# Performance work log

Hardware: AMD Instinct MI355X
Metric: run time of the kernel (lower is better)

Reference implementation:

```python
import jax, jax.numpy as jnp
import numpy as np

N_NODES = 65536
IN_CH = 512
HIDDEN = 256          # hidden_channels[0] == encoder_hidden
OUT_CH = 8
NUM_GRAPHS = 32
MAX_LEN = 4096        # static pad bound (>= max per-graph length)
BN_EPS = 1e-5


def _make_batch_ids():
    # deterministic ragged per-graph lengths summing exactly to N_NODES
    rng = np.random.RandomState(0)
    d = rng.randint(-512, 512, size=NUM_GRAPHS)
    d[-1] -= d.sum()
    lengths = N_NODES // NUM_GRAPHS + d          # each in ~[1536, 2560] <= MAX_LEN
    return jnp.asarray(np.repeat(np.arange(NUM_GRAPHS), lengths), dtype=jnp.int32)


def setup_inputs() -> dict:
    key = jax.random.key(0)
    ks = jax.random.split(key, 12)
    f32 = jnp.float32
    inp = {
        'x_res': jax.random.normal(ks[0], (N_NODES, IN_CH), dtype=f32),
        'batch': _make_batch_ids(),
        # BatchNorm1d affine params
        'bn_gamma': jnp.ones((IN_CH,), f32),
        'bn_beta': jnp.zeros((IN_CH,), f32),
        # input2transformer: Linear(C,2H) GELU Linear(2H,H) GELU Linear(H,H)
        'W1': jax.random.normal(ks[1], (IN_CH, 2 * HIDDEN), f32) * (1.0 / np.sqrt(IN_CH)),
        'b1': jnp.zeros((2 * HIDDEN,), f32),
        'W2': jax.random.normal(ks[2], (2 * HIDDEN, HIDDEN), f32) * (1.0 / np.sqrt(2 * HIDDEN)),
        'b2': jnp.zeros((HIDDEN,), f32),
        'W3': jax.random.normal(ks[3], (HIDDEN, HIDDEN), f32) * (1.0 / np.sqrt(HIDDEN)),
        'b3': jnp.zeros((HIDDEN,), f32),
        # out_angles: Linear(encoder_hidden, out_ch) GELU DynamicTanh Tanh
        'Wo': jax.random.normal(ks[4], (HIDDEN, OUT_CH), f32) * (1.0 / np.sqrt(HIDDEN)),
        'bo': jnp.zeros((OUT_CH,), f32),
        'dyt_alpha': jnp.asarray(0.5, f32),
        'dyt_w': jnp.ones((OUT_CH,), f32),
        'dyt_b': jnp.zeros((OUT_CH,), f32),
    }
    return inp


def _forward(x_res, batch, bn_gamma, bn_beta, W1, b1, W2, b2, W3, b3,
             Wo, bo, dyt_alpha, dyt_w, dyt_b):
    # BatchNorm1d (training-mode batch stats, biased var), dropout is identity (eval)
    mu = jnp.mean(x_res, axis=0)
    var = jnp.mean((x_res - mu) ** 2, axis=0)
    x = (x_res - mu) * jax.lax.rsqrt(var + BN_EPS) * bn_gamma + bn_beta
    # input2transformer MLP (torch GELU default = exact erf)
    gelu = lambda t: jax.nn.gelu(t, approximate=False)
    x = gelu(x @ W1 + b1)
    x = gelu(x @ W2 + b2)
    x = x @ W3 + b3                                   # [N, HIDDEN]
    # ragged -> padded: scatter each node into (graph, position-in-graph)
    counts = jax.ops.segment_sum(jnp.ones_like(batch, dtype=jnp.int32), batch,
                                 num_segments=NUM_GRAPHS)
    offsets = jnp.concatenate([jnp.zeros((1,), jnp.int32),
                               jnp.cumsum(counts)[:-1].astype(jnp.int32)])
    pos = jnp.arange(N_NODES, dtype=jnp.int32) - offsets[batch]
    x_pad = jnp.zeros((NUM_GRAPHS, MAX_LEN, HIDDEN), x.dtype).at[batch, pos].set(x)
    z = jnp.transpose(x_pad, (1, 0, 2))               # [MAX_LEN, NUM_GRAPHS, HIDDEN] (stack dim=1)
    # out_angles head: Linear -> GELU -> DynamicTanh -> Tanh
    a = gelu(z @ Wo + bo)
    a = dyt_w * jnp.tanh(dyt_alpha * a) + dyt_b       # DynamicTanh (channels_last)
    return jnp.tanh(a)                                # [MAX_LEN, NUM_GRAPHS, OUT_CH]


def reference(x_res, batch, bn_gamma, bn_beta, W1, b1, W2, b2, W3, b3,
              Wo, bo, dyt_alpha, dyt_w, dyt_b):
    return _forward(x_res, batch, bn_gamma, bn_beta, W1, b1, W2, b2, W3, b3,
                    Wo, bo, dyt_alpha, dyt_w, dyt_b)
```

## Files before the change

kernel.cpp:

```cpp
#include <hip/hip_runtime.h>
#include <hip/hip_bf16.h>

#define N_NODES 65536
#define IN_CH 512
#define HIDDEN 256
#define OUT_CH 8
#define NUM_GRAPHS 32
#define MAX_LEN 4096
#define BN_EPS 1e-5f
#define BN_BLOCKS 2048

using short8  = __attribute__((ext_vector_type(8))) short;
using floatx4 = __attribute__((ext_vector_type(4))) float;
typedef unsigned int u32;
typedef unsigned short u16;

__device__ inline u16 f2b(float f) {
    u32 u = __float_as_uint(f);
    u += 0x7FFFu + ((u >> 16) & 1u);
    return (u16)(u >> 16);
}
__device__ inline float gelu_f(float x) {
    float z = x + 0.044715f * x * x * x;
    float e = __builtin_exp2f(-2.3022078f * z);
    return x * __builtin_amdgcn_rcpf(1.0f + e);
}
__device__ inline float tanh_f(float y) {
    y = fminf(fmaxf(y, -20.0f), 20.0f);
    float t = __builtin_exp2f(2.885390082f * y);
    return (t - 1.0f) * __builtin_amdgcn_rcpf(t + 1.0f);
}
__device__ inline void load_lds16(const void* g, void* l) {
    __builtin_amdgcn_global_load_lds(
        (const __attribute__((address_space(1))) u32*)g,
        (__attribute__((address_space(3))) u32*)l, 16, 0, 0);
}

__global__ __launch_bounds__(256) void statscast_k(const float* __restrict__ x,
                                                   u16* __restrict__ xb,
                                                   float4* __restrict__ partials) {
    __shared__ float4 sS[128];
    __shared__ float4 sQ[128];
    int tid = threadIdx.x;
    int half = tid >> 7;
    int c = tid & 127;
    const float4* x4 = (const float4*)x;
    uint2* xb2 = (uint2*)xb;
    float4 s = make_float4(0.f, 0.f, 0.f, 0.f);
    float4 q = make_float4(0.f, 0.f, 0.f, 0.f);
    int row0 = blockIdx.x * 32;
#pragma unroll
    for (int r = half; r < 32; r += 2) {
        size_t off = (size_t)(row0 + r) * 128 + c;
        float4 v = x4[off];
        s.x += v.x; s.y += v.y; s.z += v.z; s.w += v.w;
        q.x += v.x * v.x; q.y += v.y * v.y; q.z += v.z * v.z; q.w += v.w * v.w;
        uint2 o;
        o.x = (u32)f2b(v.x) | ((u32)f2b(v.y) << 16);
        o.y = (u32)f2b(v.z) | ((u32)f2b(v.w) << 16);
        xb2[off] = o;
    }
    if (half == 1) { sS[c] = s; sQ[c] = q; }
    __syncthreads();
    if (half == 0) {
        float4 s2 = sS[c], q2 = sQ[c];
        s.x += s2.x; s.y += s2.y; s.z += s2.z; s.w += s2.w;
        q.x += q2.x; q.y += q2.y; q.z += q2.z; q.w += q2.w;
        partials[(size_t)blockIdx.x * 256 + c * 2]     = make_float4(s.x, q.x, s.y, q.y);
        partials[(size_t)blockIdx.x * 256 + c * 2 + 1] = make_float4(s.z, q.z, s.w, q.w);
    }
}

__global__ __launch_bounds__(256) void bn_reduce_k(const float4* __restrict__ partials,
                                                   const float* __restrict__ gamma,
                                                   const float* __restrict__ beta,
                                                   float* __restrict__ scale,
                                                   float* __restrict__ shift) {
    __shared__ float4 sd[256];
    int tid = threadIdx.x;
    int g = blockIdx.x;
    float4 a = make_float4(0.f, 0.f, 0.f, 0.f);
    for (int r = tid; r < BN_BLOCKS; r += 256) {
        float4 v = partials[(size_t)r * 256 + g];
        a.x += v.x; a.y += v.y; a.z += v.z; a.w += v.w;
    }
    sd[tid] = a;
    __syncthreads();
    for (int st = 128; st > 0; st >>= 1) {
        if (tid < st) {
            float4 b = sd[tid + st];
            float4 m = sd[tid];
            m.x += b.x; m.y += b.y; m.z += b.z; m.w += b.w;
            sd[tid] = m;
        }
        __syncthreads();
    }
    if (tid == 0) {
        float4 t = sd[0];
        int c0 = g * 2, c1 = g * 2 + 1;
        const float inv = 1.0f / N_NODES;
        float mu0 = t.x * inv, var0 = t.y * inv - mu0 * mu0;
        float mu1 = t.z * inv, var1 = t.w * inv - mu1 * mu1;
        float sc0 = gamma[c0] * rsqrtf(var0 + BN_EPS);
        float sc1 = gamma[c1] * rsqrtf(var1 + BN_EPS);
        scale[c0] = sc0; shift[c0] = beta[c0] - mu0 * sc0;
        scale[c1] = sc1; shift[c1] = beta[c1] - mu1 * sc1;
    }
}

__global__ __launch_bounds__(256) void prep_k(const float* __restrict__ W1,
                                              const float* __restrict__ W2,
                                              const float* __restrict__ W3,
                                              const float* __restrict__ b1,
                                              const float* __restrict__ scale,
                                              const float* __restrict__ shift,
                                              u16* __restrict__ W1T,
                                              u16* __restrict__ W2T,
                                              u16* __restrict__ W3T,
                                              float* __restrict__ b1f,
                                              const int* __restrict__ batch,
                                              int* __restrict__ offsets,
                                              const float* __restrict__ bo,
                                              const float* __restrict__ alpha_p,
                                              const float* __restrict__ dyt_w,
                                              const float* __restrict__ dyt_b,
                                              float* __restrict__ out) {
    __shared__ int sof2[NUM_GRAPHS + 1];
    int bid = blockIdx.x;
    int tid = threadIdx.x;
    if (bid < 1792) {
        int idx = bid * 256 + tid;
        if (idx < 262144) {
            int k = idx >> 9, m = idx & 511;
            W1T[(size_t)m * 512 + k] = f2b(scale[k] * W1[idx]);
        } else if (idx < 262144 + 131072) {
            int i = idx - 262144;
            int k = i >> 8, m = i & 255;
            W2T[(size_t)m * 512 + k] = f2b(W2[i]);
        } else {
            int i = idx - 393216;
            int k = i >> 8, m = i & 255;
            W3T[(size_t)m * 256 + k] = f2b(W3[i]);
        }
        if (bid == 0 && tid < NUM_GRAPHS + 1) {
            int gph = tid;
            int lo = 0, hi = N_NODES;
            while (lo < hi) {
                int mid = (lo + hi) >> 1;
                if (batch[mid] < gph) lo = mid + 1; else hi = mid;
            }
            offsets[gph] = lo;
        }
    } else if (bid < 1794) {
        int m = (bid - 1792) * 256 + tid;
        float acc = b1[m];
#pragma unroll 16
        for (int k = 0; k < 512; ++k) acc += shift[k] * W1[k * 512 + m];
        b1f[m] = acc;
    } else {
        if (tid < NUM_GRAPHS + 1) {
            int target = tid;
            int lo = 0, hi = N_NODES;
            while (lo < hi) {
                int mid = (lo + hi) >> 1;
                if (batch[mid] < target) lo = mid + 1; else hi = mid;
            }
            sof2[tid] = lo;
        }
        __syncthreads();
        int idx = (bid - 1794) * 256 + tid;
        int g = idx & 31;
        int p = idx >> 5;
        if (p >= sof2[g + 1] - sof2[g]) {
            float alpha = alpha_p[0];
            float rv[8];
#pragma unroll
            for (int c = 0; c < 8; ++c) {
                float a = gelu_f(bo[c]);
                a = dyt_w[c] * tanh_f(alpha * a) + dyt_b[c];
                rv[c] = tanh_f(a);
            }
            float4* o = (float4*)(out + (size_t)idx * OUT_CH);
            o[0] = make_float4(rv[0], rv[1], rv[2], rv[3]);
            o[1] = make_float4(rv[4], rv[5], rv[6], rv[7]);
        }
    }
}

template <int DO_GELU, int NXB>
__global__ __launch_bounds__(512) void gemm_bt_k(const u16* __restrict__ A,
                                                 const u16* __restrict__ BT,
                                                 const float* __restrict__ bias,
                                                 u16* __restrict__ C,
                                                 int K, int M) {
    __shared__ __align__(16) u16 As[256 * 64];
    __shared__ __align__(16) u16 Bs[128 * 64];
    int tid = threadIdx.x;
    int lane = tid & 63;
    int bid = blockIdx.x;
    int xcd = bid & 7;
    int slot = bid >> 3;
    int rloc = slot / NXB;
    int colb = slot - rloc * NXB;
    int row0 = (xcd * 32 + rloc) * 256;
    int col0 = colb * 128;
    int wave = tid >> 6;
    int wr = (wave >> 1) * 64;
    int wc = (wave & 1) * 64;
    int l15 = lane & 15;
    int q = lane >> 4;

    floatx4 acc[4][4] = {};

    const int nkt = K >> 6;
    for (int kt = 0; kt < nkt; ++kt) {
        int k0 = kt << 6;
#pragma unroll
        for (int s = 0; s < 4; ++s) {
            int li = s * 512 + tid;
            int r = li >> 3;
            int g = li & 7;
            int gs = g ^ (r & 7);
            load_lds16(&A[(size_t)(row0 + r) * K + k0 + gs * 8], &As[li * 8]);
        }
#pragma unroll
        for (int s = 0; s < 2; ++s) {
            int li = s * 512 + tid;
            int r = li >> 3;
            int g = li & 7;
            int gs = g ^ (r & 7);
            load_lds16(&BT[(size_t)(col0 + r) * K + k0 + gs * 8], &Bs[li * 8]);
        }
        __syncthreads();
#pragma unroll
        for (int ks = 0; ks < 2; ++ks) {
            int gidx = ks * 4 + q;
            short8 af[4], bg[4];
#pragma unroll
            for (int i = 0; i < 4; ++i) {
                int row = wr + i * 16 + l15;
                af[i] = *(const short8*)&As[row * 64 + (gidx ^ (row & 7)) * 8];
            }
#pragma unroll
            for (int j = 0; j < 4; ++j) {
                int row = wc + j * 16 + l15;
                bg[j] = *(const short8*)&Bs[row * 64 + (gidx ^ (row & 7)) * 8];
            }
#pragma unroll
            for (int i = 0; i < 4; ++i)
#pragma unroll
                for (int j = 0; j < 4; ++j)
                    acc[i][j] = __builtin_amdgcn_mfma_f32_16x16x32_bf16(bg[j], af[i], acc[i][j], 0, 0, 0);
        }
        __syncthreads();
    }
#pragma unroll
    for (int i = 0; i < 4; ++i) {
        size_t rbase = (size_t)(row0 + wr + i * 16 + l15) * M;
#pragma unroll
        for (int j = 0; j < 4; ++j) {
            int c = col0 + wc + j * 16 + q * 4;
            float4 b4 = *(const float4*)&bias[c];
            float v0 = acc[i][j][0] + b4.x;
            float v1 = acc[i][j][1] + b4.y;
            float v2 = acc[i][j][2] + b4.z;
            float v3 = acc[i][j][3] + b4.w;
            if (DO_GELU) { v0 = gelu_f(v0); v1 = gelu_f(v1); v2 = gelu_f(v2); v3 = gelu_f(v3); }
            uint2 pk;
            pk.x = (u32)f2b(v0) | ((u32)f2b(v1) << 16);
            pk.y = (u32)f2b(v2) | ((u32)f2b(v3) << 16);
            *(uint2*)&C[rbase + c] = pk;
        }
    }
}

#define FENCE asm volatile("" ::: "memory")

__global__ __launch_bounds__(512, 2) void gemm23h_k(const u16* __restrict__ A,
                                                    const u16* __restrict__ B2T,
                                                    const float* __restrict__ b2v,
                                                    const u16* __restrict__ W3T,
                                                    const float* __restrict__ b3v,
                                                    const float* __restrict__ Wo,
                                                    const float* __restrict__ bo,
                                                    const int* __restrict__ offsets,
                                                    const float* __restrict__ alpha_p,
                                                    const float* __restrict__ dyt_w,
                                                    const float* __restrict__ dyt_b,
                                                    float* __restrict__ out) {
    __shared__ __align__(16) u16 lds[65536];
    __shared__ float sWo[HIDDEN * OUT_CH];
    __shared__ int soff[NUM_GRAPHS + 1];
    int tid = threadIdx.x;
    int lane = tid & 63;
    int bid = blockIdx.x;
    int xcd = bid & 7;
    int slot = bid >> 3;
    int row0 = (xcd * 32 + slot) * 256;
    int wave = tid >> 6;
    int wr = (wave >> 2) * 128;
    int wc = (wave & 3) * 64;
    int l15 = lane & 15;
    int q = lane >> 4;

    ((float4*)sWo)[tid] = ((const float4*)Wo)[tid];
    if (tid < NUM_GRAPHS + 1) soff[tid] = offsets[tid];

    floatx4 acc[8][4] = {};

    const u16* pA[4];
    const u16* pB[4];
    int ldst[4];
#pragma unroll
    for (int s = 0; s < 4; ++s) {
        int li = s * 512 + tid;
        int r = li >> 3;
        int g = li & 7;
        int gs = g ^ (r & 7);
        pA[s] = A + (size_t)(row0 + r) * 512 + gs * 8;
        pB[s] = B2T + (size_t)r * 512 + gs * 8;
        ldst[s] = li * 8;
    }

#define LDA2(BASE, GIDX)                                                             \
    _Pragma("unroll")                                                                \
    for (int i = 0; i < 4; ++i) {                                                    \
        int row = (BASE) + i * 16 + l15;                                             \
        af[i] = *(const short8*)&lds[curA + row * 64 + (((GIDX) ^ (row & 7)) << 3)]; \
    }
#define LDB2(BASE, GIDX)                                                             \
    _Pragma("unroll")                                                                \
    for (int j = 0; j < 4; ++j) {                                                    \
        int row = (BASE) + j * 16 + l15;                                             \
        bg[j] = *(const short8*)&lds[curB + row * 64 + (((GIDX) ^ (row & 7)) << 3)]; \
    }
#define MFMA16(IB)                                                                   \
    __builtin_amdgcn_s_setprio(1);                                                   \
    _Pragma("unroll")                                                                \
    for (int i = 0; i < 4; ++i)                                                      \
        _Pragma("unroll")                                                            \
        for (int j = 0; j < 4; ++j)                                                  \
            acc[(IB) + i][j] = __builtin_amdgcn_mfma_f32_16x16x32_bf16(              \
                bg[j], af[i], acc[(IB) + i][j], 0, 0, 0);                            \
    __builtin_amdgcn_s_setprio(0)

#pragma unroll
    for (int s = 0; s < 4; ++s) load_lds16(pA[s], &lds[ldst[s]]);
#pragma unroll
    for (int s = 0; s < 4; ++s) load_lds16(pB[s], &lds[32768 + ldst[s]]);

    const int nt = 8;
    for (int t = 0; t < nt; ++t) {
        const int cur = t & 1;
        const int nx = cur ^ 1;
        const bool last = (t + 1 == nt);
        const int kn = (t + 1) << 6;
        const int curA = cur * 16384, curB = 32768 + cur * 16384;
        const int nxA = nx * 16384,  nxB = 32768 + nx * 16384;
        short8 af[4], bg[4];

        if (!last) {
            load_lds16(pA[0] + kn, &lds[nxA + ldst[0]]);
            load_lds16(pA[1] + kn, &lds[nxA + ldst[1]]);
        }
        if (last) asm volatile("s_waitcnt vmcnt(0)" ::: "memory");
        else      asm volatile("s_waitcnt vmcnt(2)" ::: "memory");
        __builtin_amdgcn_s_barrier();
        FENCE;
        LDA2(wr, q);
        LDB2(wc, q);
        MFMA16(0);
        FENCE;
        __builtin_amdgcn_s_barrier();
        LDA2(wr + 64, q);
        if (!last) {
            load_lds16(pA[2] + kn, &lds[nxA + ldst[2]]);
            load_lds16(pA[3] + kn, &lds[nxA + ldst[3]]);
        }
        FENCE;
        __builtin_amdgcn_s_barrier();
        FENCE;
        MFMA16(4);
        FENCE;
        __builtin_amdgcn_s_barrier();
        LDA2(wr, 4 + q);
        LDB2(wc, 4 + q);
        if (!last) {
            load_lds16(pB[0] + kn, &lds[nxB + ldst[0]]);
            load_lds16(pB[1] + kn, &lds[nxB + ldst[1]]);
        }
        FENCE;
        __builtin_amdgcn_s_barrier();
        FENCE;
        MFMA16(0);
        FENCE;
        __builtin_amdgcn_s_barrier();
        LDA2(wr + 64, 4 + q);
        if (!last) {
            load_lds16(pB[2] + kn, &lds[nxB + ldst[2]]);
            load_lds16(pB[3] + kn, &lds[nxB + ldst[3]]);
        }
        FENCE;
        __builtin_amdgcn_s_barrier();
        FENCE;
        MFMA16(4);
        FENCE;
        __builtin_amdgcn_s_barrier();
        FENCE;
    }
    __syncthreads();

#pragma unroll
    for (int i = 0; i < 8; ++i) {
        int row = wr + i * 16 + l15;
#pragma unroll
        for (int j = 0; j < 4; ++j) {
            int c = wc + j * 16 + q * 4;
            float4 b4 = *(const float4*)&b2v[c];
            float v0 = gelu_f(acc[i][j][0] + b4.x);
            float v1 = gelu_f(acc[i][j][1] + b4.y);
            float v2 = gelu_f(acc[i][j][2] + b4.z);
            float v3 = gelu_f(acc[i][j][3] + b4.w);
            uint2 pk;
            pk.x = (u32)f2b(v0) | ((u32)f2b(v1) << 16);
            pk.y = (u32)f2b(v2) | ((u32)f2b(v3) << 16);
            int gr = c >> 3;
            int addr = row * 256 + ((gr ^ (row & 7)) << 3) + (q & 1) * 4;
            *(uint2*)&lds[addr] = pk;
        }
    }
    __syncthreads();

#pragma unroll
    for (int i = 0; i < 8; ++i)
#pragma unroll
        for (int j = 0; j < 4; ++j)
            acc[i][j] = (floatx4){0.f, 0.f, 0.f, 0.f};

    for (int ks = 0; ks < 8; ++ks) {
        int gidx = ks * 4 + q;
        short8 af[8], bg[4];
#pragma unroll
        for (int j = 0; j < 4; ++j) {
            int colr = wc + j * 16 + l15;
            bg[j] = *(const short8*)&W3T[(size_t)colr * 256 + gidx * 8];
        }
#pragma unroll
        for (int i = 0; i < 8; ++i) {
            int row = wr + i * 16 + l15;
            af[i] = *(const short8*)&lds[row * 256 + ((gidx ^ (row & 7)) << 3)];
        }
        __builtin_amdgcn_s_setprio(1);
#pragma unroll
        for (int i = 0; i < 8; ++i)
#pragma unroll
            for (int j = 0; j < 4; ++j)
                acc[i][j] = __builtin_amdgcn_mfma_f32_16x16x32_bf16(bg[j], af[i], acc[i][j], 0, 0, 0);
        __builtin_amdgcn_s_setprio(0);
    }
    __syncthreads();

#pragma unroll
    for (int i = 0; i < 8; ++i) {
        int row = wr + i * 16 + l15;
#pragma unroll
        for (int j = 0; j < 4; ++j) {
            int c = wc + j * 16 + q * 4;
            float4 b4 = *(const float4*)&b3v[c];
            float v0 = acc[i][j][0] + b4.x;
            float v1 = acc[i][j][1] + b4.y;
            float v2 = acc[i][j][2] + b4.z;
            float v3 = acc[i][j][3] + b4.w;
            uint2 pk;
            pk.x = (u32)f2b(v0) | ((u32)f2b(v1) << 16);
            pk.y = (u32)f2b(v2) | ((u32)f2b(v3) << 16);
            int gr = c >> 3;
            int addr = row * 256 + ((gr ^ (row & 31)) << 3) + (q & 1) * 4;
            *(uint2*)&lds[addr] = pk;
        }
    }
    __syncthreads();

    {
        int r = tid >> 1;
        int chalf = (tid & 1) * 4;
        int n = row0 + r;
        int lo = 0, hi = NUM_GRAPHS;
        while (hi - lo > 1) {
            int mid = (lo + hi) >> 1;
            if (soff[mid] <= n) lo = mid; else hi = mid;
        }
        int g = lo;
        int p = n - soff[g];
        float4 a4 = *(const float4*)&bo[chalf];
#pragma unroll 4
        for (int kk = 0; kk < 32; ++kk) {
            short8 h = *(const short8*)&lds[r * 256 + ((kk ^ (r & 31)) << 3)];
#pragma unroll
            for (int e = 0; e < 8; ++e) {
                float hv = __uint_as_float((u32)(u16)h[e] << 16);
                const float* w = &sWo[(kk * 8 + e) * 8 + chalf];
                a4.x += hv * w[0];
                a4.y += hv * w[1];
                a4.z += hv * w[2];
                a4.w += hv * w[3];
            }
        }
        float alpha = alpha_p[0];
        float av[4] = {a4.x, a4.y, a4.z, a4.w};
        float rv[4];
#pragma unroll
        for (int c = 0; c < 4; ++c) {
            float a = gelu_f(av[c]);
            a = dyt_w[chalf + c] * tanh_f(alpha * a) + dyt_b[chalf + c];
            rv[c] = tanh_f(a);
        }
        *(float4*)&out[((size_t)(p * NUM_GRAPHS + g)) * 8 + chalf] =
            make_float4(rv[0], rv[1], rv[2], rv[3]);
    }
#undef LDA2
#undef LDB2
#undef MFMA16
}

extern "C" void kernel_launch(void* const* d_in, const int* in_sizes, int n_in,
                              void* d_out, int out_size, void* d_ws, size_t ws_size,
                              hipStream_t stream) {
    (void)in_sizes; (void)n_in; (void)out_size; (void)ws_size;
    const float* x_res = (const float*)d_in[0];
    const int*   batch = (const int*)d_in[1];
    const float* gamma = (const float*)d_in[2];
    const float* beta  = (const float*)d_in[3];
    const float* W1    = (const float*)d_in[4];
    const float* b1    = (const float*)d_in[5];
    const float* W2    = (const float*)d_in[6];
    const float* b2    = (const float*)d_in[7];
    const float* W3    = (const float*)d_in[8];
    const float* b3    = (const float*)d_in[9];
    const float* Wo    = (const float*)d_in[10];
    const float* bo    = (const float*)d_in[11];
    const float* alpha = (const float*)d_in[12];
    const float* dyt_w = (const float*)d_in[13];
    const float* dyt_b = (const float*)d_in[14];
    float* out = (float*)d_out;

    char* ws = (char*)d_ws;
    float* scale = (float*)(ws + 0);
    float* shift = (float*)(ws + 2048);
    float* b1f   = (float*)(ws + 4096);
    int*   offs  = (int*)(ws + 8192);
    u16* W1T = (u16*)(ws + 16384);
    u16* W2T = (u16*)(ws + 16384 + 524288);
    u16* W3T = (u16*)(ws + 16384 + 524288 + 262144);
    const size_t MB = 1024 * 1024;
    u16* xb = (u16*)(ws + 2 * MB);
    u16* h1 = (u16*)(ws + 66 * MB);
    float4* partials = (float4*)(ws + 66 * MB);

    statscast_k<<<BN_BLOCKS, 256, 0, stream>>>(x_res, xb, partials);
    bn_reduce_k<<<256, 256, 0, stream>>>(partials, gamma, beta, scale, shift);
    prep_k<<<2306, 256, 0, stream>>>(W1, W2, W3, b1, scale, shift,
                                     W1T, W2T, W3T, b1f, batch, offs,
                                     bo, alpha, dyt_w, dyt_b, out);
    gemm_bt_k<1, 4><<<1024, 512, 0, stream>>>(xb, W1T, b1f, h1, 512, 512);
    gemm23h_k<<<256, 512, 0, stream>>>(h1, W2T, b2, W3T, b3, Wo, bo, offs,
                                       alpha, dyt_w, dyt_b, out);
}
```

Before: 353.2 us.

## Rewrite first GEMM with 256x256 tiles and double-buffered LDS prefetch pipeline

The first MLP GEMM (x@W1 with GELU) moves from a 256x128 tile with a single LDS buffer to a 256x256 tile with double-buffered LDS. Global-to-LDS loads for the next K tile are interleaved with MFMA phases using explicit waitcnt, barriers and setprio. This targets exposed global load latency and gives each block more operand reuse. In exchange it uses 128KB of LDS and 32 accumulators per thread, halves the grid to 512 blocks, and adds more barriers per K step.

```diff
diff --git a/kernel.cpp b/kernel.cpp
--- a/kernel.cpp
+++ b/kernel.cpp
@@ -187,14 +187,16 @@
     }
 }
 
+#define FENCE asm volatile("" ::: "memory")
+
 template <int DO_GELU, int NXB>
-__global__ __launch_bounds__(512) void gemm_bt_k(const u16* __restrict__ A,
-                                                 const u16* __restrict__ BT,
-                                                 const float* __restrict__ bias,
-                                                 u16* __restrict__ C,
-                                                 int K, int M) {
-    __shared__ __align__(16) u16 As[256 * 64];
-    __shared__ __align__(16) u16 Bs[128 * 64];
+__global__ __launch_bounds__(512, 2) void gemm_bt8_k(const u16* __restrict__ A,
+                                                     const u16* __restrict__ BT,
+                                                     const float* __restrict__ bias,
+                                                     u16* __restrict__ C,
+                                                     int K, int M) {
+    __shared__ __align__(16) u16 As[2][256 * 64];
+    __shared__ __align__(16) u16 Bs[2][256 * 64];
     int tid = threadIdx.x;
     int lane = tid & 63;
     int bid = blockIdx.x;
@@ -203,59 +205,107 @@
     int rloc = slot / NXB;
     int colb = slot - rloc * NXB;
     int row0 = (xcd * 32 + rloc) * 256;
-    int col0 = colb * 128;
+    int col0 = colb * 256;
     int wave = tid >> 6;
-    int wr = (wave >> 1) * 64;
-    int wc = (wave & 1) * 64;
+    int wr = (wave >> 2) * 128;
+    int wc = (wave & 3) * 64;
     int l15 = lane & 15;
     int q = lane >> 4;
 
-    floatx4 acc[4][4] = {};
-
-    const int nkt = K >> 6;
-    for (int kt = 0; kt < nkt; ++kt) {
-        int k0 = kt << 6;
-#pragma unroll
-        for (int s = 0; s < 4; ++s) {
-            int li = s * 512 + tid;
-            int r = li >> 3;
-            int g = li & 7;
-            int gs = g ^ (r & 7);
-            load_lds16(&A[(size_t)(row0 + r) * K + k0 + gs * 8], &As[li * 8]);
-        }
-#pragma unroll
-        for (int s = 0; s < 2; ++s) {
-            int li = s * 512 + tid;
-            int r = li >> 3;
-            int g = li & 7;
-            int gs = g ^ (r & 7);
-            load_lds16(&BT[(size_t)(col0 + r) * K + k0 + gs * 8], &Bs[li * 8]);
-        }
-        __syncthreads();
-#pragma unroll
-        for (int ks = 0; ks < 2; ++ks) {
-            int gidx = ks * 4 + q;
-            short8 af[4], bg[4];
-#pragma unroll
-            for (int i = 0; i < 4; ++i) {
-                int row = wr + i * 16 + l15;
-                af[i] = *(const short8*)&As[row * 64 + (gidx ^ (row & 7)) * 8];
-            }
-#pragma unroll
-            for (int j = 0; j < 4; ++j) {
-                int row = wc + j * 16 + l15;
-                bg[j] = *(const short8*)&Bs[row * 64 + (gidx ^ (row & 7)) * 8];
-            }
-#pragma unroll
-            for (int i = 0; i < 4; ++i)
-#pragma unroll
-                for (int j = 0; j < 4; ++j)
-                    acc[i][j] = __builtin_amdgcn_mfma_f32_16x16x32_bf16(bg[j], af[i], acc[i][j], 0, 0, 0);
-        }
-        __syncthreads();
-    }
-#pragma unroll
-    for (int i = 0; i < 4; ++i) {
+    floatx4 acc[8][4] = {};
+
+    const u16* pA[4];
+    const u16* pB[4];
+    int ldst[4];
+#pragma unroll
+    for (int s = 0; s < 4; ++s) {
+        int li = s * 512 + tid;
+        int r = li >> 3;
+        int g = li & 7;
+        int gs = g ^ (r & 7);
+        pA[s] = A + (size_t)(row0 + r) * K + gs * 8;
+        pB[s] = BT + (size_t)(col0 + r) * K + gs * 8;
+        ldst[s] = li * 8;
+    }
+
+#define LOAD_AF(BASE, GIDX)                                                    \
+    _Pragma("unroll")                                                          \
+    for (int i = 0; i < 4; ++i) {                                              \
+        int row = (BASE) + i * 16 + l15;                                       \
+        af[i] = *(const short8*)&As[cur][row * 64 + ((GIDX) ^ (row & 7)) * 8]; \
+    }
+#define LOAD_BG(BASE, GIDX)                                                    \
+    _Pragma("unroll")                                                          \
+    for (int j = 0; j < 4; ++j) {                                              \
+        int row = (BASE) + j * 16 + l15;                                       \
+        bg[j] = *(const short8*)&Bs[cur][row * 64 + ((GIDX) ^ (row & 7)) * 8]; \
+    }
+#define MFMA16(IB)                                                             \
+    __builtin_amdgcn_s_setprio(1);                                             \
+    _Pragma("unroll")                                                          \
+    for (int i = 0; i < 4; ++i)                                                \
+        _Pragma("unroll")                                                      \
+        for (int j = 0; j < 4; ++j)                                            \
+            acc[(IB) + i][j] = __builtin_amdgcn_mfma_f32_16x16x32_bf16(        \
+                bg[j], af[i], acc[(IB) + i][j], 0, 0, 0);                      \
+    __builtin_amdgcn_s_setprio(0)
+
+#pragma unroll
+    for (int s = 0; s < 4; ++s) load_lds16(pA[s], &As[0][ldst[s]]);
+#pragma unroll
+    for (int s = 0; s < 4; ++s) load_lds16(pB[s], &Bs[0][ldst[s]]);
+
+    const int nt = K >> 6;
+    for (int t = 0; t < nt; ++t) {
+        const int cur = t & 1;
+        const int nx = cur ^ 1;
+        const int kn = (t + 1 < nt) ? ((t + 1) << 6) : 0;
+        short8 af[4], bg[4];
+
+        load_lds16(pA[0] + kn, &As[nx][ldst[0]]);
+        load_lds16(pA[1] + kn, &As[nx][ldst[1]]);
+        asm volatile("s_waitcnt vmcnt(2)" ::: "memory");
+        __builtin_amdgcn_s_barrier();
+        FENCE;
+        LOAD_AF(wr, q);
+        LOAD_BG(wc, q);
+        MFMA16(0);
+        FENCE;
+        __builtin_amdgcn_s_barrier();
+        LOAD_AF(wr + 64, q);
+        load_lds16(pA[2] + kn, &As[nx][ldst[2]]);
+        load_lds16(pA[3] + kn, &As[nx][ldst[3]]);
+        FENCE;
+        __builtin_amdgcn_s_barrier();
+        FENCE;
+        MFMA16(4);
+        FENCE;
+        __builtin_amdgcn_s_barrier();
+        LOAD_AF(wr, 4 + q);
+        LOAD_BG(wc, 4 + q);
+        load_lds16(pB[0] + kn, &Bs[nx][ldst[0]]);
+        load_lds16(pB[1] + kn, &Bs[nx][ldst[1]]);
+        FENCE;
+        __builtin_amdgcn_s_barrier();
+        FENCE;
+        MFMA16(0);
+        FENCE;
+        __builtin_amdgcn_s_barrier();
+        LOAD_AF(wr + 64, 4 + q);
+        load_lds16(pB[2] + kn, &Bs[nx][ldst[2]]);
+        load_lds16(pB[3] + kn, &Bs[nx][ldst[3]]);
+        FENCE;
+        __builtin_amdgcn_s_barrier();
+        FENCE;
+        MFMA16(4);
+        FENCE;
+        __builtin_amdgcn_s_barrier();
+        FENCE;
+    }
+    asm volatile("s_waitcnt vmcnt(0)" ::: "memory");
+
+#pragma unroll
+    for (int i = 0; i < 8; ++i) {
         size_t rbase = (size_t)(row0 + wr + i * 16 + l15) * M;
 #pragma unroll
         for (int j = 0; j < 4; ++j) {
@@ -272,9 +322,10 @@
             *(uint2*)&C[rbase + c] = pk;
         }
     }
-}
-
-#define FENCE asm volatile("" ::: "memory")
+#undef LOAD_AF
+#undef LOAD_BG
+#undef MFMA16
+}
 
 __global__ __launch_bounds__(512, 2) void gemm23h_k(const u16* __restrict__ A,
                                                     const u16* __restrict__ B2T,
@@ -562,7 +613,7 @@
     prep_k<<<2306, 256, 0, stream>>>(W1, W2, W3, b1, scale, shift,
                                      W1T, W2T, W3T, b1f, batch, offs,
                                      bo, alpha, dyt_w, dyt_b, out);
-    gemm_bt_k<1, 4><<<1024, 512, 0, stream>>>(xb, W1T, b1f, h1, 512, 512);
+    gemm_bt8_k<1, 2><<<512, 512, 0, stream>>>(xb, W1T, b1f, h1, 512, 512);
     gemm23h_k<<<256, 512, 0, stream>>>(h1, W2T, b2, W3T, b3, Wo, bo, offs,
                                        alpha, dyt_w, dyt_b, out);
 }
```

New measurement: 366.0 us. 1.04x slower.

## Redistribute prep work across stats and BN-reduce kernels, shrink prep to tiny b1f kernel

Applied to the files above, without the earlier changes.

Moves the W2/W3 transposition, the offset search and the padding-output fill into extra blocks of the stats/cast kernel so they run alongside the large streaming pass. W1 scaling and transposition now happen inside the BN reduce kernel, one channel pair per block, and the old prep kernel becomes a two-block kernel that only computes the folded bias. This shortens the serial chain of wide launches before the first GEMM. In exchange, the W1T writes in bn_reduce are strided and uncoalesced, and the b1f kernel stays a serial 512-step loop.

```diff
diff --git a/kernel.cpp b/kernel.cpp
--- a/kernel.cpp
+++ b/kernel.cpp
@@ -38,45 +38,108 @@
 
 __global__ __launch_bounds__(256) void statscast_k(const float* __restrict__ x,
                                                    u16* __restrict__ xb,
-                                                   float4* __restrict__ partials) {
+                                                   float4* __restrict__ partials,
+                                                   const float* __restrict__ W2,
+                                                   const float* __restrict__ W3,
+                                                   u16* __restrict__ W2T,
+                                                   u16* __restrict__ W3T,
+                                                   const int* __restrict__ batch,
+                                                   int* __restrict__ offsets,
+                                                   const float* __restrict__ bo,
+                                                   const float* __restrict__ alpha_p,
+                                                   const float* __restrict__ dyt_w,
+                                                   const float* __restrict__ dyt_b,
+                                                   float* __restrict__ out) {
     __shared__ float4 sS[128];
     __shared__ float4 sQ[128];
+    __shared__ int sof2[NUM_GRAPHS + 1];
     int tid = threadIdx.x;
-    int half = tid >> 7;
-    int c = tid & 127;
-    const float4* x4 = (const float4*)x;
-    uint2* xb2 = (uint2*)xb;
-    float4 s = make_float4(0.f, 0.f, 0.f, 0.f);
-    float4 q = make_float4(0.f, 0.f, 0.f, 0.f);
-    int row0 = blockIdx.x * 32;
-#pragma unroll
-    for (int r = half; r < 32; r += 2) {
-        size_t off = (size_t)(row0 + r) * 128 + c;
-        float4 v = x4[off];
-        s.x += v.x; s.y += v.y; s.z += v.z; s.w += v.w;
-        q.x += v.x * v.x; q.y += v.y * v.y; q.z += v.z * v.z; q.w += v.w * v.w;
-        uint2 o;
-        o.x = (u32)f2b(v.x) | ((u32)f2b(v.y) << 16);
-        o.y = (u32)f2b(v.z) | ((u32)f2b(v.w) << 16);
-        xb2[off] = o;
-    }
-    if (half == 1) { sS[c] = s; sQ[c] = q; }
-    __syncthreads();
-    if (half == 0) {
-        float4 s2 = sS[c], q2 = sQ[c];
-        s.x += s2.x; s.y += s2.y; s.z += s2.z; s.w += s2.w;
-        q.x += q2.x; q.y += q2.y; q.z += q2.z; q.w += q2.w;
-        partials[(size_t)blockIdx.x * 256 + c * 2]     = make_float4(s.x, q.x, s.y, q.y);
-        partials[(size_t)blockIdx.x * 256 + c * 2 + 1] = make_float4(s.z, q.z, s.w, q.w);
+    int bid = blockIdx.x;
+    if (bid < 2048) {
+        int half = tid >> 7;
+        int c = tid & 127;
+        const float4* x4 = (const float4*)x;
+        uint2* xb2 = (uint2*)xb;
+        float4 s = make_float4(0.f, 0.f, 0.f, 0.f);
+        float4 q = make_float4(0.f, 0.f, 0.f, 0.f);
+        int row0 = bid * 32;
+#pragma unroll
+        for (int r = half; r < 32; r += 2) {
+            size_t off = (size_t)(row0 + r) * 128 + c;
+            float4 v = x4[off];
+            s.x += v.x; s.y += v.y; s.z += v.z; s.w += v.w;
+            q.x += v.x * v.x; q.y += v.y * v.y; q.z += v.z * v.z; q.w += v.w * v.w;
+            uint2 o;
+            o.x = (u32)f2b(v.x) | ((u32)f2b(v.y) << 16);
+            o.y = (u32)f2b(v.z) | ((u32)f2b(v.w) << 16);
+            xb2[off] = o;
+        }
+        if (half == 1) { sS[c] = s; sQ[c] = q; }
+        __syncthreads();
+        if (half == 0) {
+            float4 s2 = sS[c], q2 = sQ[c];
+            s.x += s2.x; s.y += s2.y; s.z += s2.z; s.w += s2.w;
+            q.x += q2.x; q.y += q2.y; q.z += q2.z; q.w += q2.w;
+            partials[(size_t)bid * 256 + c * 2]     = make_float4(s.x, q.x, s.y, q.y);
+            partials[(size_t)bid * 256 + c * 2 + 1] = make_float4(s.z, q.z, s.w, q.w);
+        }
+    } else if (bid < 2560) {
+        int i = (bid - 2048) * 256 + tid;
+        int k = i >> 8, m = i & 255;
+        W2T[(size_t)m * 512 + k] = f2b(W2[i]);
+    } else if (bid < 2816) {
+        int i = (bid - 2560) * 256 + tid;
+        int k = i >> 8, m = i & 255;
+        W3T[(size_t)m * 256 + k] = f2b(W3[i]);
+    } else if (bid < 3328) {
+        if (tid < NUM_GRAPHS + 1) {
+            int target = tid;
+            int lo = 0, hi = N_NODES;
+            while (lo < hi) {
+                int mid = (lo + hi) >> 1;
+                if (batch[mid] < target) lo = mid + 1; else hi = mid;
+            }
+            sof2[tid] = lo;
+        }
+        __syncthreads();
+        int idx = (bid - 2816) * 256 + tid;
+        int g = idx & 31;
+        int p = idx >> 5;
+        if (p >= sof2[g + 1] - sof2[g]) {
+            float alpha = alpha_p[0];
+            float rv[8];
+#pragma unroll
+            for (int c = 0; c < 8; ++c) {
+                float a = gelu_f(bo[c]);
+                a = dyt_w[c] * tanh_f(alpha * a) + dyt_b[c];
+                rv[c] = tanh_f(a);
+            }
+            float4* o = (float4*)(out + (size_t)idx * OUT_CH);
+            o[0] = make_float4(rv[0], rv[1], rv[2], rv[3]);
+            o[1] = make_float4(rv[4], rv[5], rv[6], rv[7]);
+        }
+    } else {
+        if (tid < NUM_GRAPHS + 1) {
+            int gph = tid;
+            int lo = 0, hi = N_NODES;
+            while (lo < hi) {
+                int mid = (lo + hi) >> 1;
+                if (batch[mid] < gph) lo = mid + 1; else hi = mid;
+            }
+            offsets[gph] = lo;
+        }
     }
 }
 
 __global__ __launch_bounds__(256) void bn_reduce_k(const float4* __restrict__ partials,
                                                    const float* __restrict__ gamma,
                                                    const float* __restrict__ beta,
+                                                   const float* __restrict__ W1,
                                                    float* __restrict__ scale,
-                                                   float* __restrict__ shift) {
+                                                   float* __restrict__ shift,
+                                                   u16* __restrict__ W1T) {
     __shared__ float4 sd[256];
+    __shared__ float ssc[2];
     int tid = threadIdx.x;
     int g = blockIdx.x;
     float4 a = make_float4(0.f, 0.f, 0.f, 0.f);
@@ -95,9 +158,9 @@
         }
         __syncthreads();
     }
+    int c0 = g * 2, c1 = g * 2 + 1;
     if (tid == 0) {
         float4 t = sd[0];
-        int c0 = g * 2, c1 = g * 2 + 1;
         const float inv = 1.0f / N_NODES;
         float mu0 = t.x * inv, var0 = t.y * inv - mu0 * mu0;
         float mu1 = t.z * inv, var1 = t.w * inv - mu1 * mu1;
@@ -105,86 +168,26 @@
         float sc1 = gamma[c1] * rsqrtf(var1 + BN_EPS);
         scale[c0] = sc0; shift[c0] = beta[c0] - mu0 * sc0;
         scale[c1] = sc1; shift[c1] = beta[c1] - mu1 * sc1;
-    }
-}
-
-__global__ __launch_bounds__(256) void prep_k(const float* __restrict__ W1,
-                                              const float* __restrict__ W2,
-                                              const float* __restrict__ W3,
-                                              const float* __restrict__ b1,
-                                              const float* __restrict__ scale,
-                                              const float* __restrict__ shift,
-                                              u16* __restrict__ W1T,
-                                              u16* __restrict__ W2T,
-                                              u16* __restrict__ W3T,
-                                              float* __restrict__ b1f,
-                                              const int* __restrict__ batch,
-                                              int* __restrict__ offsets,
-                                              const float* __restrict__ bo,
-                                              const float* __restrict__ alpha_p,
-                                              const float* __restrict__ dyt_w,
-                                              const float* __restrict__ dyt_b,
-                                              float* __restrict__ out) {
-    __shared__ int sof2[NUM_GRAPHS + 1];
-    int bid = blockIdx.x;
-    int tid = threadIdx.x;
-    if (bid < 1792) {
-        int idx = bid * 256 + tid;
-        if (idx < 262144) {
-            int k = idx >> 9, m = idx & 511;
-            W1T[(size_t)m * 512 + k] = f2b(scale[k] * W1[idx]);
-        } else if (idx < 262144 + 131072) {
-            int i = idx - 262144;
-            int k = i >> 8, m = i & 255;
-            W2T[(size_t)m * 512 + k] = f2b(W2[i]);
-        } else {
-            int i = idx - 393216;
-            int k = i >> 8, m = i & 255;
-            W3T[(size_t)m * 256 + k] = f2b(W3[i]);
-        }
-        if (bid == 0 && tid < NUM_GRAPHS + 1) {
-            int gph = tid;
-            int lo = 0, hi = N_NODES;
-            while (lo < hi) {
-                int mid = (lo + hi) >> 1;
-                if (batch[mid] < gph) lo = mid + 1; else hi = mid;
-            }
-            offsets[gph] = lo;
-        }
-    } else if (bid < 1794) {
-        int m = (bid - 1792) * 256 + tid;
-        float acc = b1[m];
+        ssc[0] = sc0; ssc[1] = sc1;
+    }
+    __syncthreads();
+    float s0 = ssc[0], s1 = ssc[1];
+#pragma unroll
+    for (int mm = tid; mm < 512; mm += 256) {
+        W1T[(size_t)mm * 512 + c0] = f2b(s0 * W1[(size_t)c0 * 512 + mm]);
+        W1T[(size_t)mm * 512 + c1] = f2b(s1 * W1[(size_t)c1 * 512 + mm]);
+    }
+}
+
+__global__ __launch_bounds__(256) void b1f_k(const float* __restrict__ W1,
+                                             const float* __restrict__ b1,
+                                             const float* __restrict__ shift,
+                                             float* __restrict__ b1f) {
+    int m = blockIdx.x * 256 + threadIdx.x;
+    float acc = b1[m];
 #pragma unroll 16
-        for (int k = 0; k < 512; ++k) acc += shift[k] * W1[k * 512 + m];
-        b1f[m] = acc;
-    } else {
-        if (tid < NUM_GRAPHS + 1) {
-            int target = tid;
-            int lo = 0, hi = N_NODES;
-            while (lo < hi) {
-                int mid = (lo + hi) >> 1;
-                if (batch[mid] < target) lo = mid + 1; else hi = mid;
-            }
-            sof2[tid] = lo;
-        }
-        __syncthreads();
-        int idx = (bid - 1794) * 256 + tid;
-        int g = idx & 31;
-        int p = idx >> 5;
-        if (p >= sof2[g + 1] - sof2[g]) {
-            float alpha = alpha_p[0];
-            float rv[8];
-#pragma unroll
-            for (int c = 0; c < 8; ++c) {
-                float a = gelu_f(bo[c]);
-                a = dyt_w[c] * tanh_f(alpha * a) + dyt_b[c];
-                rv[c] = tanh_f(a);
-            }
-            float4* o = (float4*)(out + (size_t)idx * OUT_CH);
-            o[0] = make_float4(rv[0], rv[1], rv[2], rv[3]);
-            o[1] = make_float4(rv[4], rv[5], rv[6], rv[7]);
-        }
-    }
+    for (int k = 0; k < 512; ++k) acc += shift[k] * W1[k * 512 + m];
+    b1f[m] = acc;
 }
 
 template <int DO_GELU, int NXB>
@@ -557,11 +560,10 @@
     u16* h1 = (u16*)(ws + 66 * MB);
     float4* partials = (float4*)(ws + 66 * MB);
 
-    statscast_k<<<BN_BLOCKS, 256, 0, stream>>>(x_res, xb, partials);
-    bn_reduce_k<<<256, 256, 0, stream>>>(partials, gamma, beta, scale, shift);
-    prep_k<<<2306, 256, 0, stream>>>(W1, W2, W3, b1, scale, shift,
-                                     W1T, W2T, W3T, b1f, batch, offs,
-                                     bo, alpha, dyt_w, dyt_b, out);
+    statscast_k<<<3329, 256, 0, stream>>>(x_res, xb, partials, W2, W3, W2T, W3T,
+                                          batch, offs, bo, alpha, dyt_w, dyt_b, out);
+    bn_reduce_k<<<256, 256, 0, stream>>>(partials, gamma, beta, W1, scale, shift, W1T);
+    b1f_k<<<2, 256, 0, stream>>>(W1, b1, shift, b1f);
     gemm_bt_k<1, 4><<<1024, 512, 0, stream>>>(xb, W1T, b1f, h1, 512, 512);
     gemm23h_k<<<256, 512, 0, stream>>>(h1, W2T, b2, W3T, b3, Wo, bo, offs,
                                        alpha, dyt_w, dyt_b, out);
```

New measurement: 361.0 us. 2.2% more time.

## Halve fused GEMM2/3 row tile, drop software pipeline, raise occupancy

Applied to the files above, without the earlier changes.

The fused GEMM2+GEMM3+head kernel now processes 128 rows per block instead of 256, launching 512 blocks with half the LDS and accumulator registers, and sets launch bounds to allow four blocks per CU. The hand-scheduled double-buffered K loop with split barriers and priority hints is replaced by a simple single-buffered load/sync/compute loop. The head epilogue assigns four threads per row with two output channels each. The intent is more parallelism and occupancy to hide latency, at the cost of losing explicit load/compute overlap and re-reading W2 twice as often.

```diff
diff --git a/kernel.cpp b/kernel.cpp
--- a/kernel.cpp
+++ b/kernel.cpp
@@ -274,9 +274,7 @@
     }
 }
 
-#define FENCE asm volatile("" ::: "memory")
-
-__global__ __launch_bounds__(512, 2) void gemm23h_k(const u16* __restrict__ A,
+__global__ __launch_bounds__(512, 4) void gemm23h_k(const u16* __restrict__ A,
                                                     const u16* __restrict__ B2T,
                                                     const float* __restrict__ b2v,
                                                     const u16* __restrict__ W3T,
@@ -288,7 +286,7 @@
                                                     const float* __restrict__ dyt_w,
                                                     const float* __restrict__ dyt_b,
                                                     float* __restrict__ out) {
-    __shared__ __align__(16) u16 lds[65536];
+    __shared__ __align__(16) u16 lds[32768];
     __shared__ float sWo[HIDDEN * OUT_CH];
     __shared__ int soff[NUM_GRAPHS + 1];
     int tid = threadIdx.x;
@@ -296,9 +294,9 @@
     int bid = blockIdx.x;
     int xcd = bid & 7;
     int slot = bid >> 3;
-    int row0 = (xcd * 32 + slot) * 256;
+    int row0 = (xcd * 64 + slot) * 128;
     int wave = tid >> 6;
-    int wr = (wave >> 2) * 128;
+    int wr = (wave >> 2) * 64;
     int wc = (wave & 3) * 64;
     int l15 = lane & 15;
     int q = lane >> 4;
@@ -306,112 +304,62 @@
     ((float4*)sWo)[tid] = ((const float4*)Wo)[tid];
     if (tid < NUM_GRAPHS + 1) soff[tid] = offsets[tid];
 
-    floatx4 acc[8][4] = {};
-
-    const u16* pA[4];
+    floatx4 acc[4][4] = {};
+
+    const u16* pA[2];
     const u16* pB[4];
-    int ldst[4];
+    int ldstA[2], ldstB[4];
+#pragma unroll
+    for (int s = 0; s < 2; ++s) {
+        int li = s * 512 + tid;
+        int r = li >> 3;
+        int g = li & 7;
+        int gs = g ^ (r & 7);
+        pA[s] = A + (size_t)(row0 + r) * 512 + gs * 8;
+        ldstA[s] = li * 8;
+    }
 #pragma unroll
     for (int s = 0; s < 4; ++s) {
         int li = s * 512 + tid;
         int r = li >> 3;
         int g = li & 7;
         int gs = g ^ (r & 7);
-        pA[s] = A + (size_t)(row0 + r) * 512 + gs * 8;
         pB[s] = B2T + (size_t)r * 512 + gs * 8;
-        ldst[s] = li * 8;
-    }
-
-#define LDA2(BASE, GIDX)                                                             \
-    _Pragma("unroll")                                                                \
-    for (int i = 0; i < 4; ++i) {                                                    \
-        int row = (BASE) + i * 16 + l15;                                             \
-        af[i] = *(const short8*)&lds[curA + row * 64 + (((GIDX) ^ (row & 7)) << 3)]; \
-    }
-#define LDB2(BASE, GIDX)                                                             \
-    _Pragma("unroll")                                                                \
-    for (int j = 0; j < 4; ++j) {                                                    \
-        int row = (BASE) + j * 16 + l15;                                             \
-        bg[j] = *(const short8*)&lds[curB + row * 64 + (((GIDX) ^ (row & 7)) << 3)]; \
-    }
-#define MFMA16(IB)                                                                   \
-    __builtin_amdgcn_s_setprio(1);                                                   \
-    _Pragma("unroll")                                                                \
-    for (int i = 0; i < 4; ++i)                                                      \
-        _Pragma("unroll")                                                            \
-        for (int j = 0; j < 4; ++j)                                                  \
-            acc[(IB) + i][j] = __builtin_amdgcn_mfma_f32_16x16x32_bf16(              \
-                bg[j], af[i], acc[(IB) + i][j], 0, 0, 0);                            \
-    __builtin_amdgcn_s_setprio(0)
-
-#pragma unroll
-    for (int s = 0; s < 4; ++s) load_lds16(pA[s], &lds[ldst[s]]);
-#pragma unroll
-    for (int s = 0; s < 4; ++s) load_lds16(pB[s], &lds[32768 + ldst[s]]);
-
-    const int nt = 8;
-    for (int t = 0; t < nt; ++t) {
-        const int cur = t & 1;
-        const int nx = cur ^ 1;
-        const bool last = (t + 1 == nt);
-        const int kn = (t + 1) << 6;
-        const int curA = cur * 16384, curB = 32768 + cur * 16384;
-        const int nxA = nx * 16384,  nxB = 32768 + nx * 16384;
-        short8 af[4], bg[4];
-
-        if (!last) {
-            load_lds16(pA[0] + kn, &lds[nxA + ldst[0]]);
-            load_lds16(pA[1] + kn, &lds[nxA + ldst[1]]);
-        }
-        if (last) asm volatile("s_waitcnt vmcnt(0)" ::: "memory");
-        else      asm volatile("s_waitcnt vmcnt(2)" ::: "memory");
-        __builtin_amdgcn_s_barrier();
-        FENCE;
-        LDA2(wr, q);
-        LDB2(wc, q);
-        MFMA16(0);
-        FENCE;
-        __builtin_amdgcn_s_barrier();
-        LDA2(wr + 64, q);
-        if (!last) {
-            load_lds16(pA[2] + kn, &lds[nxA + ldst[2]]);
-            load_lds16(pA[3] + kn, &lds[nxA + ldst[3]]);
-        }
-        FENCE;
-        __builtin_amdgcn_s_barrier();
-        FENCE;
-        MFMA16(4);
-        FENCE;
-        __builtin_amdgcn_s_barrier();
-        LDA2(wr, 4 + q);
-        LDB2(wc, 4 + q);
-        if (!last) {
-            load_lds16(pB[0] + kn, &lds[nxB + ldst[0]]);
-            load_lds16(pB[1] + kn, &lds[nxB + ldst[1]]);
-        }
-        FENCE;
-        __builtin_amdgcn_s_barrier();
-        FENCE;
-        MFMA16(0);
-        FENCE;
-        __builtin_amdgcn_s_barrier();
-        LDA2(wr + 64, 4 + q);
-        if (!last) {
-            load_lds16(pB[2] + kn, &lds[nxB + ldst[2]]);
-            load_lds16(pB[3] + kn, &lds[nxB + ldst[3]]);
-        }
-        FENCE;
-        __builtin_amdgcn_s_barrier();
-        FENCE;
-        MFMA16(4);
-        FENCE;
-        __builtin_amdgcn_s_barrier();
-        FENCE;
-    }
-    __syncthreads();
-
-#pragma unroll
-    for (int i = 0; i < 8; ++i) {
+        ldstB[s] = 8192 + li * 8;
+    }
+
+    for (int kt = 0; kt < 8; ++kt) {
+        int k0 = kt << 6;
+#pragma unroll
+        for (int s = 0; s < 2; ++s) load_lds16(pA[s] + k0, &lds[ldstA[s]]);
+#pragma unroll
+        for (int s = 0; s < 4; ++s) load_lds16(pB[s] + k0, &lds[ldstB[s]]);
+        __syncthreads();
+#pragma unroll
+        for (int ks = 0; ks < 2; ++ks) {
+            int gidx = ks * 4 + q;
+            short8 af[4], bg[4];
+#pragma unroll
+            for (int i = 0; i < 4; ++i) {
+                int row = wr + i * 16 + l15;
+                af[i] = *(const short8*)&lds[row * 64 + ((gidx ^ (row & 7)) << 3)];
+            }
+#pragma unroll
+            for (int j = 0; j < 4; ++j) {
+                int brow = wc + j * 16 + l15;
+                bg[j] = *(const short8*)&lds[8192 + brow * 64 + ((gidx ^ (brow & 7)) << 3)];
+            }
+#pragma unroll
+            for (int i = 0; i < 4; ++i)
+#pragma unroll
+                for (int j = 0; j < 4; ++j)
+                    acc[i][j] = __builtin_amdgcn_mfma_f32_16x16x32_bf16(bg[j], af[i], acc[i][j], 0, 0, 0);
+        }
+        __syncthreads();
+    }
+
+#pragma unroll
+    for (int i = 0; i < 4; ++i) {
         int row = wr + i * 16 + l15;
 #pragma unroll
         for (int j = 0; j < 4; ++j) {
@@ -432,27 +380,27 @@
     __syncthreads();
 
 #pragma unroll
-    for (int i = 0; i < 8; ++i)
+    for (int i = 0; i < 4; ++i)
 #pragma unroll
         for (int j = 0; j < 4; ++j)
             acc[i][j] = (floatx4){0.f, 0.f, 0.f, 0.f};
 
     for (int ks = 0; ks < 8; ++ks) {
         int gidx = ks * 4 + q;
-        short8 af[8], bg[4];
+        short8 af[4], bg[4];
 #pragma unroll
         for (int j = 0; j < 4; ++j) {
             int colr = wc + j * 16 + l15;
             bg[j] = *(const short8*)&W3T[(size_t)colr * 256 + gidx * 8];
         }
 #pragma unroll
-        for (int i = 0; i < 8; ++i) {
+        for (int i = 0; i < 4; ++i) {
             int row = wr + i * 16 + l15;
             af[i] = *(const short8*)&lds[row * 256 + ((gidx ^ (row & 7)) << 3)];
         }
         __builtin_amdgcn_s_setprio(1);
 #pragma unroll
-        for (int i = 0; i < 8; ++i)
+        for (int i = 0; i < 4; ++i)
 #pragma unroll
             for (int j = 0; j < 4; ++j)
                 acc[i][j] = __builtin_amdgcn_mfma_f32_16x16x32_bf16(bg[j], af[i], acc[i][j], 0, 0, 0);
@@ -461,7 +409,7 @@
     __syncthreads();
 
 #pragma unroll
-    for (int i = 0; i < 8; ++i) {
+    for (int i = 0; i < 4; ++i) {
         int row = wr + i * 16 + l15;
 #pragma unroll
         for (int j = 0; j < 4; ++j) {
@@ -482,8 +430,8 @@
     __syncthreads();
 
     {
-        int r = tid >> 1;
-        int chalf = (tid & 1) * 4;
+        int r = tid >> 2;
+        int cq = (tid & 3) * 2;
         int n = row0 + r;
         int lo = 0, hi = NUM_GRAPHS;
         while (hi - lo > 1) {
@@ -492,35 +440,29 @@
         }
         int g = lo;
         int p = n - soff[g];
-        float4 a4 = *(const float4*)&bo[chalf];
+        float a0 = bo[cq], a1 = bo[cq + 1];
 #pragma unroll 4
         for (int kk = 0; kk < 32; ++kk) {
             short8 h = *(const short8*)&lds[r * 256 + ((kk ^ (r & 31)) << 3)];
 #pragma unroll
             for (int e = 0; e < 8; ++e) {
                 float hv = __uint_as_float((u32)(u16)h[e] << 16);
-                const float* w = &sWo[(kk * 8 + e) * 8 + chalf];
-                a4.x += hv * w[0];
-                a4.y += hv * w[1];
-                a4.z += hv * w[2];
-                a4.w += hv * w[3];
+                const float* w = &sWo[(kk * 8 + e) * 8 + cq];
+                a0 += hv * w[0];
+                a1 += hv * w[1];
             }
         }
         float alpha = alpha_p[0];
-        float av[4] = {a4.x, a4.y, a4.z, a4.w};
-        float rv[4];
-#pragma unroll
-        for (int c = 0; c < 4; ++c) {
+        float av[2] = {a0, a1};
+        float rv[2];
+#pragma unroll
+        for (int c = 0; c < 2; ++c) {
             float a = gelu_f(av[c]);
-            a = dyt_w[chalf + c] * tanh_f(alpha * a) + dyt_b[chalf + c];
+            a = dyt_w[cq + c] * tanh_f(alpha * a) + dyt_b[cq + c];
             rv[c] = tanh_f(a);
         }
-        *(float4*)&out[((size_t)(p * NUM_GRAPHS + g)) * 8 + chalf] =
-            make_float4(rv[0], rv[1], rv[2], rv[3]);
-    }
-#undef LDA2
-#undef LDB2
-#undef MFMA16
+        *(float2*)&out[((size_t)(p * NUM_GRAPHS + g)) * 8 + cq] = make_float2(rv[0], rv[1]);
+    }
 }
 
 extern "C" void kernel_launch(void* const* d_in, const int* in_sizes, int n_in,
@@ -563,6 +505,6 @@
                                      W1T, W2T, W3T, b1f, batch, offs,
                                      bo, alpha, dyt_w, dyt_b, out);
     gemm_bt_k<1, 4><<<1024, 512, 0, stream>>>(xb, W1T, b1f, h1, 512, 512);
-    gemm23h_k<<<256, 512, 0, stream>>>(h1, W2T, b2, W3T, b3, Wo, bo, offs,
+    gemm23h_k<<<512, 512, 0, stream>>>(h1, W2T, b2, W3T, b3, Wo, bo, offs,
                                        alpha, dyt_w, dyt_b, out);
 }
```

Result: no change. 348.6 us (-1.3%).
